# Optimization experiments

Measured on AMD Instinct MI355X. Metric: run time of the kernel, lower is better.

Reference implementation:

```python
import jax, jax.numpy as jnp
import numpy as np

D_IN = 512
N_EXPERTS = 32
HID = 16
BATCH = 262144


def setup_inputs() -> dict:
    key = jax.random.key(0)
    kx, kg, k1, kb1, k2, kb2 = jax.random.split(key, 6)
    x = jax.random.normal(kx, (BATCH, D_IN), dtype=jnp.float32)
    # gating: n_experts independent Linear(d_in, 1, bias=False) -> [E, d_in]
    Wg = jax.random.normal(kg, (N_EXPERTS, D_IN), dtype=jnp.float32) * 0.02
    # experts: Linear(d_in,16) -> GELU -> Linear(16,1)
    W1 = jax.random.normal(k1, (N_EXPERTS, D_IN, HID), dtype=jnp.float32) * 0.02
    b1 = jax.random.normal(kb1, (N_EXPERTS, HID), dtype=jnp.float32) * 0.02
    W2 = jax.random.normal(k2, (N_EXPERTS, HID), dtype=jnp.float32) * 0.02
    b2 = jax.random.normal(kb2, (N_EXPERTS,), dtype=jnp.float32) * 0.02
    return {"x": x, "Wg": Wg, "W1": W1, "b1": b1, "W2": W2, "b2": b2}


def reference(x, Wg, W1, b1, W2, b2):
    # gating scores for all experts at once: [B, E]
    gating = jnp.einsum("bd,ed->be", x, Wg)
    gate = jax.nn.softmax(gating, axis=1)  # softmax over experts (torch dim=1)
    # all experts' first layer in one batched GEMM: [B, E, HID]
    h = jax.nn.gelu(jnp.einsum("bd,edh->beh", x, W1) + b1, approximate=False)
    # second layer collapses HID -> scalar per expert: [B, E]
    out = jnp.einsum("beh,eh->be", h, W2) + b2
    # bmm([B,1,E],[B,E,1]) == weighted sum over experts -> [B, 1]
    xi = jnp.sum(out * gate, axis=1, keepdims=True)
    return xi
```

## Files before the change

kernel.cpp:

```cpp
#include <hip/hip_runtime.h>
#include <hip/hip_bf16.h>

#define D_IN 512
#define NEXP 32
#define HID 16
#define NT 34
#define KSTEPS 16
#define BM 128
#define NW 8
#define BATCH 262144
#define LDGX 129

typedef __attribute__((ext_vector_type(8))) short bfrag;
typedef __attribute__((ext_vector_type(4))) float f32x4;

__device__ inline ushort f2bf(float f) {
  uint32_t u = __float_as_uint(f);
  u += 0x7fffu + ((u >> 16) & 1u);
  return (ushort)(u >> 16);
}

__device__ inline bfrag cvt8(const float4 a, const float4 b) {
  union { bfrag v; uint u[4]; } r;
  asm("v_cvt_pk_bf16_f32 %0, %1, %2" : "=v"(r.u[0]) : "v"(a.x), "v"(a.y));
  asm("v_cvt_pk_bf16_f32 %0, %1, %2" : "=v"(r.u[1]) : "v"(a.z), "v"(a.w));
  asm("v_cvt_pk_bf16_f32 %0, %1, %2" : "=v"(r.u[2]) : "v"(b.x), "v"(b.y));
  asm("v_cvt_pk_bf16_f32 %0, %1, %2" : "=v"(r.u[3]) : "v"(b.z), "v"(b.w));
  return r.v;
}

__device__ inline float gelu_t(float v) {
  float t = 0.7978845608028654f * fmaf(0.044715f * v * v, v, v);
  t = fminf(fmaxf(t, -9.f), 9.f);
  float e = __expf(-2.f * t);
  float th = (1.f - e) * __builtin_amdgcn_rcpf(1.f + e);
  return 0.5f * v * (1.f + th);
}

__device__ inline void gload_lds16(const ushort* g, ushort* l) {
  __builtin_amdgcn_global_load_lds(
      (const __attribute__((address_space(1))) void*)g,
      (__attribute__((address_space(3))) void*)l, 16, 0, 0);
}

__global__ void prepack_kernel(const float* __restrict__ Wg,
                               const float* __restrict__ W1,
                               ushort* __restrict__ P) {
  int tid = blockIdx.x * 256 + threadIdx.x;
  const int total = KSTEPS * NT * 64;
  if (tid >= total) return;
  int l  = tid & 63;
  int t  = (tid >> 6) % NT;
  int ks = tid / (NT * 64);
  int n  = t * 16 + (l & 15);
  int kb = ks * 32 + (l >> 4) * 8;
  __align__(16) ushort v[8];
#pragma unroll
  for (int j = 0; j < 8; ++j) {
    int k = kb + j;
    float w;
    if (n < NEXP) {
      w = Wg[n * D_IN + k];
    } else {
      int e = (n - 32) >> 4, h = (n - 32) & 15;
      w = W1[(e * D_IN + k) * HID + h];
    }
    v[j] = f2bf(w);
  }
  *reinterpret_cast<int4*>(P + (size_t)tid * 8) = *reinterpret_cast<const int4*>(v);
}

__global__ __launch_bounds__(512, 2)
void moe_kernel(const float* __restrict__ x, const ushort* __restrict__ P,
                const float* __restrict__ b1, const float* __restrict__ W2,
                const float* __restrict__ b2, float* __restrict__ out) {
  __shared__ __align__(16) ushort Blds[2][NT * 512];
  __shared__ float gxl[17 * LDGX];
  __shared__ float p0l[BM];
  __shared__ float sl[BM];

  const int tid = threadIdx.x;
  const int l = tid & 63;
  const int wid = tid >> 6;
  const int wm = wid >> 1, wn = wid & 1;
  const int lane16 = l & 15, lg = l >> 4;
  const size_t rowBase = (size_t)blockIdx.x * BM;

  f32x4 acc[2][17];
#pragma unroll
  for (int f = 0; f < 2; ++f)
#pragma unroll
    for (int t = 0; t < 17; ++t) acc[f][t] = (f32x4){0.f, 0.f, 0.f, 0.f};

  const float* xp0 = x + (rowBase + wm * 32 + lane16) * D_IN + lg * 8;
  const float* xp1 = xp0 + 16 * D_IN;

  float4 abuf[2][4];

#pragma unroll
  for (int tg = wid; tg < NT; tg += NW)
    gload_lds16(P + ((size_t)tg * 64 + l) * 8, &Blds[0][tg * 512]);
  abuf[0][0] = *reinterpret_cast<const float4*>(xp0);
  abuf[0][1] = *reinterpret_cast<const float4*>(xp0 + 4);
  abuf[0][2] = *reinterpret_cast<const float4*>(xp1);
  abuf[0][3] = *reinterpret_cast<const float4*>(xp1 + 4);
  asm volatile("s_waitcnt vmcnt(4)" ::: "memory");
  __builtin_amdgcn_s_barrier();
  __builtin_amdgcn_sched_barrier(0);

#pragma unroll
  for (int ks = 0; ks < KSTEPS; ++ks) {
    const int cur = ks & 1, nxt = cur ^ 1;
    if (ks < KSTEPS - 1) {
#pragma unroll
      for (int tg = wid; tg < NT; tg += NW)
        gload_lds16(P + ((size_t)((ks + 1) * NT + tg) * 64 + l) * 8,
                    &Blds[nxt][tg * 512]);
      abuf[nxt][0] = *reinterpret_cast<const float4*>(xp0 + (ks + 1) * 32);
      abuf[nxt][1] = *reinterpret_cast<const float4*>(xp0 + (ks + 1) * 32 + 4);
      abuf[nxt][2] = *reinterpret_cast<const float4*>(xp1 + (ks + 1) * 32);
      abuf[nxt][3] = *reinterpret_cast<const float4*>(xp1 + (ks + 1) * 32 + 4);
    }
    const bfrag a0 = cvt8(abuf[cur][0], abuf[cur][1]);
    const bfrag a1 = cvt8(abuf[cur][2], abuf[cur][3]);
#pragma unroll
    for (int t = 0; t < 17; ++t) {
      const bfrag b = *reinterpret_cast<const bfrag*>(&Blds[cur][(wn * 17 + t) * 512 + l * 8]);
      acc[0][t] = __builtin_amdgcn_mfma_f32_16x16x32_bf16(b, a0, acc[0][t], 0, 0, 0);
      acc[1][t] = __builtin_amdgcn_mfma_f32_16x16x32_bf16(b, a1, acc[1][t], 0, 0, 0);
    }
    if (ks < KSTEPS - 1) {
      asm volatile("s_waitcnt vmcnt(4)" ::: "memory");
      __builtin_amdgcn_s_barrier();
      __builtin_amdgcn_sched_barrier(0);
    }
  }

  const int row0 = wm * 32 + lane16;
  float oreg[17][2];

  if (wn == 0) {
    float gh[2][8];
    float pac[2] = {0.f, 0.f};
#pragma unroll
    for (int f = 0; f < 2; ++f) {
      const int row = row0 + f * 16;
      float mx = fmaxf(fmaxf(fmaxf(acc[f][0][0], acc[f][0][1]), fmaxf(acc[f][0][2], acc[f][0][3])),
                       fmaxf(fmaxf(acc[f][1][0], acc[f][1][1]), fmaxf(acc[f][1][2], acc[f][1][3])));
      mx = fmaxf(mx, __shfl_xor(mx, 16));
      mx = fmaxf(mx, __shfl_xor(mx, 32));
      float sum = 0.f;
#pragma unroll
      for (int t = 0; t < 2; ++t)
#pragma unroll
        for (int r = 0; r < 4; ++r) {
          float g = __expf(acc[f][t][r] - mx);
          gh[f][t * 4 + r] = g;
          sum += g;
        }
      sum += __shfl_xor(sum, 16);
      sum += __shfl_xor(sum, 32);
      if (lg == 0) sl[row] = sum;
      if (lg == 3) gxl[row] = gh[f][3];
#pragma unroll
      for (int r = 0; r < 4; ++r)
        gxl[(1 + lg * 4 + r) * LDGX + row] = gh[f][4 + r];
    }
#pragma unroll
    for (int t = 2; t < 17; ++t) {
      const int e = t - 2;
      const float4 b1v = *reinterpret_cast<const float4*>(b1 + e * HID + lg * 4);
      const float4 w2v = *reinterpret_cast<const float4*>(W2 + e * HID + lg * 4);
      const float b2v = b2[e];
#pragma unroll
      for (int f = 0; f < 2; ++f) {
        float p = gelu_t(acc[f][t][0] + b1v.x) * w2v.x;
        p = fmaf(gelu_t(acc[f][t][1] + b1v.y), w2v.y, p);
        p = fmaf(gelu_t(acc[f][t][2] + b1v.z), w2v.z, p);
        p = fmaf(gelu_t(acc[f][t][3] + b1v.w), w2v.w, p);
        p += __shfl_xor(p, 16);
        p += __shfl_xor(p, 32);
        if (lg == (e >> 2)) pac[f] = fmaf(p + b2v, gh[f][e & 3], pac[f]);
      }
    }
#pragma unroll
    for (int f = 0; f < 2; ++f) {
      float p0 = pac[f];
      p0 += __shfl_xor(p0, 16);
      p0 += __shfl_xor(p0, 32);
      if (lg == 0) p0l[row0 + f * 16] = p0;
    }
  } else {
#pragma unroll
    for (int t = 0; t < 17; ++t) {
      const int e = t + 15;
      const float4 b1v = *reinterpret_cast<const float4*>(b1 + e * HID + lg * 4);
      const float4 w2v = *reinterpret_cast<const float4*>(W2 + e * HID + lg * 4);
      const float b2v = b2[e];
#pragma unroll
      for (int f = 0; f < 2; ++f) {
        float p = gelu_t(acc[f][t][0] + b1v.x) * w2v.x;
        p = fmaf(gelu_t(acc[f][t][1] + b1v.y), w2v.y, p);
        p = fmaf(gelu_t(acc[f][t][2] + b1v.z), w2v.z, p);
        p = fmaf(gelu_t(acc[f][t][3] + b1v.w), w2v.w, p);
        p += __shfl_xor(p, 16);
        p += __shfl_xor(p, 32);
        oreg[t][f] = p + b2v;
      }
    }
  }

  __syncthreads();
  if (wn == 1) {
#pragma unroll
    for (int f = 0; f < 2; ++f) {
      const int row = row0 + f * 16;
      float a = p0l[row];
#pragma unroll
      for (int t = 0; t < 17; ++t)
        a = fmaf(oreg[t][f], gxl[t * LDGX + row], a);
      if (lg == 0) out[rowBase + row] = a / sl[row];
    }
  }
}

extern "C" void kernel_launch(void* const* d_in, const int* in_sizes, int n_in,
                              void* d_out, int out_size, void* d_ws, size_t ws_size,
                              hipStream_t stream) {
  const float* x  = (const float*)d_in[0];
  const float* Wg = (const float*)d_in[1];
  const float* W1 = (const float*)d_in[2];
  const float* b1 = (const float*)d_in[3];
  const float* W2 = (const float*)d_in[4];
  const float* b2 = (const float*)d_in[5];
  float* out = (float*)d_out;
  ushort* P = (ushort*)d_ws;

  hipLaunchKernelGGL(prepack_kernel, dim3((KSTEPS * NT * 64 + 255) / 256), dim3(256),
                     0, stream, Wg, W1, P);
  hipLaunchKernelGGL(moe_kernel, dim3(BATCH / BM), dim3(512),
                     0, stream, x, P, b1, W2, b2, out);
}
```

Baseline: 320.2 us.

## Triple-buffer weight tiles in LDS with two-step prefetch and uniform per-wave loads

Moves the B-operand LDS staging from double to triple buffering, so weight tiles for step ks+2 are issued while step ks computes. Each wave now issues a fixed five tile loads (the 34 tiles wrap around, so some are loaded twice) instead of a variable count, which keeps vmcnt accounting uniform. The x loads stay double-buffered and the sched_barriers are removed. The cost is roughly 35KB more LDS per block, which may lower occupancy below two blocks per CU, plus redundant duplicate tile loads.

```diff
diff --git a/kernel.cpp b/kernel.cpp
--- a/kernel.cpp
+++ b/kernel.cpp
@@ -7,9 +7,9 @@
 #define NT 34
 #define KSTEPS 16
 #define BM 128
-#define NW 8
 #define BATCH 262144
 #define LDGX 129
+#define SPW 5
 
 typedef __attribute__((ext_vector_type(8))) short bfrag;
 typedef __attribute__((ext_vector_type(4))) float f32x4;
@@ -74,7 +74,7 @@
 void moe_kernel(const float* __restrict__ x, const ushort* __restrict__ P,
                 const float* __restrict__ b1, const float* __restrict__ W2,
                 const float* __restrict__ b2, float* __restrict__ out) {
-  __shared__ __align__(16) ushort Blds[2][NT * 512];
+  __shared__ __align__(16) ushort Blds[3][NT * 512];
   __shared__ float gxl[17 * LDGX];
   __shared__ float p0l[BM];
   __shared__ float sl[BM];
@@ -86,6 +86,13 @@
   const int lane16 = l & 15, lg = l >> 4;
   const size_t rowBase = (size_t)blockIdx.x * BM;
 
+  int stg[SPW];
+#pragma unroll
+  for (int i = 0; i < SPW; ++i) {
+    int t = wid * SPW + i;
+    stg[i] = (t >= NT) ? (t - NT) : t;
+  }
+
   f32x4 acc[2][17];
 #pragma unroll
   for (int f = 0; f < 2; ++f)
@@ -97,42 +104,51 @@
 
   float4 abuf[2][4];
 
-#pragma unroll
-  for (int tg = wid; tg < NT; tg += NW)
-    gload_lds16(P + ((size_t)tg * 64 + l) * 8, &Blds[0][tg * 512]);
   abuf[0][0] = *reinterpret_cast<const float4*>(xp0);
   abuf[0][1] = *reinterpret_cast<const float4*>(xp0 + 4);
   abuf[0][2] = *reinterpret_cast<const float4*>(xp1);
   abuf[0][3] = *reinterpret_cast<const float4*>(xp1 + 4);
-  asm volatile("s_waitcnt vmcnt(4)" ::: "memory");
+#pragma unroll
+  for (int g = 0; g < 2; ++g)
+#pragma unroll
+    for (int i = 0; i < SPW; ++i)
+      gload_lds16(P + ((size_t)(g * NT + stg[i]) * 64 + l) * 8,
+                  &Blds[g][stg[i] * 512]);
+  asm volatile("s_waitcnt vmcnt(5)" ::: "memory");
   __builtin_amdgcn_s_barrier();
-  __builtin_amdgcn_sched_barrier(0);
 
 #pragma unroll
   for (int ks = 0; ks < KSTEPS; ++ks) {
     const int cur = ks & 1, nxt = cur ^ 1;
+    const int rb = ks % 3;
+    const bfrag a0 = cvt8(abuf[cur][0], abuf[cur][1]);
+    const bfrag a1 = cvt8(abuf[cur][2], abuf[cur][3]);
     if (ks < KSTEPS - 1) {
-#pragma unroll
-      for (int tg = wid; tg < NT; tg += NW)
-        gload_lds16(P + ((size_t)((ks + 1) * NT + tg) * 64 + l) * 8,
-                    &Blds[nxt][tg * 512]);
       abuf[nxt][0] = *reinterpret_cast<const float4*>(xp0 + (ks + 1) * 32);
       abuf[nxt][1] = *reinterpret_cast<const float4*>(xp0 + (ks + 1) * 32 + 4);
       abuf[nxt][2] = *reinterpret_cast<const float4*>(xp1 + (ks + 1) * 32);
       abuf[nxt][3] = *reinterpret_cast<const float4*>(xp1 + (ks + 1) * 32 + 4);
     }
-    const bfrag a0 = cvt8(abuf[cur][0], abuf[cur][1]);
-    const bfrag a1 = cvt8(abuf[cur][2], abuf[cur][3]);
+    if (ks < KSTEPS - 2) {
+      const int wb = (ks + 2) % 3;
+#pragma unroll
+      for (int i = 0; i < SPW; ++i)
+        gload_lds16(P + ((size_t)((ks + 2) * NT + stg[i]) * 64 + l) * 8,
+                    &Blds[wb][stg[i] * 512]);
+    }
 #pragma unroll
     for (int t = 0; t < 17; ++t) {
-      const bfrag b = *reinterpret_cast<const bfrag*>(&Blds[cur][(wn * 17 + t) * 512 + l * 8]);
+      const bfrag b = *reinterpret_cast<const bfrag*>(
+          &Blds[rb][(wn * 17 + t) * 512 + l * 8]);
       acc[0][t] = __builtin_amdgcn_mfma_f32_16x16x32_bf16(b, a0, acc[0][t], 0, 0, 0);
       acc[1][t] = __builtin_amdgcn_mfma_f32_16x16x32_bf16(b, a1, acc[1][t], 0, 0, 0);
     }
     if (ks < KSTEPS - 1) {
-      asm volatile("s_waitcnt vmcnt(4)" ::: "memory");
+      if (ks < KSTEPS - 2)
+        asm volatile("s_waitcnt vmcnt(9)" ::: "memory");
+      else
+        asm volatile("s_waitcnt vmcnt(4)" ::: "memory");
       __builtin_amdgcn_s_barrier();
-      __builtin_amdgcn_sched_barrier(0);
     }
   }
 
```

After: 332.6 us. 1.04x slower.
